# Performance work log

Measured on AMD Instinct MI355X. Metric: run time of the kernel, lower is better.

The kernel has to match this reference:

```python
import jax, jax.numpy as jnp
import numpy as np

NUM_HEADS = 8
NUM_Q = 64
RANK = 64
DIM = 768
LN_EPS = 1e-5


def setup_inputs() -> dict:
    key = jax.random.key(0)
    ks = jax.random.split(key, 8)
    b, n = 4, 1024
    x = jax.random.normal(ks[0], (b, NUM_Q, DIM), dtype=jnp.float32)
    context = jax.random.normal(ks[1], (b, n, DIM), dtype=jnp.float32)
    s = 0.02
    Wq = jax.random.normal(ks[2], (DIM, DIM), dtype=jnp.float32) * s
    Wk = jax.random.normal(ks[3], (DIM, DIM), dtype=jnp.float32) * s
    Wv1 = jax.random.normal(ks[4], (DIM, NUM_Q * RANK), dtype=jnp.float32) * s
    ln_g = jnp.ones((NUM_Q * RANK,), dtype=jnp.float32)
    ln_b = jnp.zeros((NUM_Q * RANK,), dtype=jnp.float32)
    Wc = jax.random.normal(ks[5], (NUM_Q, RANK, DIM), dtype=jnp.float32) * s
    Wout = jax.random.normal(ks[6], (DIM, DIM), dtype=jnp.float32) * s
    return {"x": x, "context": context, "Wq": Wq, "Wk": Wk, "Wv1": Wv1,
            "ln_g": ln_g, "ln_b": ln_b, "Wc": Wc, "Wout": Wout}


def reference(x, context, Wq, Wk, Wv1, ln_g, ln_b, Wc, Wout):
    b, nq, d = x.shape
    n = context.shape[1]
    h, dh = NUM_HEADS, d // NUM_HEADS

    q = x @ Wq                      # [b, nq, d]
    k = context @ Wk                # [b, n, d]

    # q-aware V: Linear -> LayerNorm(all_q_mid) -> grouped 1x1 conv (per-query rank->d)
    h1 = context @ Wv1              # [b, n, NUM_Q*RANK]
    mu = jnp.mean(h1, axis=-1, keepdims=True)
    var = jnp.var(h1, axis=-1, keepdims=True)
    h1 = (h1 - mu) * jax.lax.rsqrt(var + LN_EPS) * ln_g + ln_b
    vmid = h1.reshape(b, n, NUM_Q, RANK)
    v = jnp.einsum('bnqr,qrd->bqnd', vmid, Wc)   # [b, NUM_Q, n, d]
    # split heads: 'b q n (h dh) -> b h q n dh'
    v = v.reshape(b, NUM_Q, n, h, dh).transpose(0, 3, 1, 2, 4)

    qh = q.reshape(b, nq, h, dh).transpose(0, 2, 1, 3)   # [b,h,nq,dh]
    kh = k.reshape(b, n, h, dh).transpose(0, 2, 1, 3)    # [b,h,n,dh]
    scale = dh ** (-0.25)
    sim = jnp.einsum('bhid,bhjd->bhij', qh * scale, kh * scale)
    attn = jax.nn.softmax(sim, axis=-1)                  # [b,h,nq,n]
    out = jnp.einsum('bhij,bhijd->bhid', attn, v)        # per-query V
    out = out.transpose(0, 2, 1, 3).reshape(b, nq, d)
    return out @ Wout
```

## Files before the change

### kernel.cpp

```cpp
#include <hip/hip_runtime.h>
#include <math.h>

typedef unsigned short ushort_t;
typedef __bf16 bf16x8 __attribute__((ext_vector_type(8)));
typedef float f32x4 __attribute__((ext_vector_type(4)));

__device__ __forceinline__ ushort_t f2b_rne(float f) {
    union { float f; unsigned int u; } c;
    c.f = f;
    unsigned int u = c.u;
    u += 0x7FFFu + ((u >> 16) & 1u);
    return (ushort_t)(u >> 16);
}
__device__ __forceinline__ float b2f(ushort_t v) {
    union { unsigned int u; float f; } c;
    c.u = ((unsigned int)v) << 16;
    return c.f;
}

__device__ __forceinline__ void gl_lds16(const ushort_t* g, ushort_t* l) {
    __builtin_amdgcn_global_load_lds(
        (const __attribute__((address_space(1))) void*)g,
        (__attribute__((address_space(3))) void*)l, 16, 0, 0);
}

__global__ __launch_bounds__(256) void prep(
    const float* __restrict__ x, const float* __restrict__ context,
    const float* __restrict__ Wq, const float* __restrict__ Wk,
    const float* __restrict__ Wv1, const float* __restrict__ Wout,
    ushort_t* __restrict__ x_b, ushort_t* __restrict__ ctx_b,
    ushort_t* __restrict__ Wq_t, ushort_t* __restrict__ Wk_t,
    ushort_t* __restrict__ Wv1_t, ushort_t* __restrict__ Wout_b,
    float* __restrict__ colzero,
    int b, int n) {
    const int t = threadIdx.x;
    const int bid = blockIdx.x;
    const int nb_x = (b * 64 * 768 / 4) / 256;
    const int nb_c = (b * n * 768 / 4) / 256;

    if (bid < nb_x + nb_c) {
        const float* in = (bid < nb_x) ? x : context;
        ushort_t* outp = (bid < nb_x) ? x_b : ctx_b;
        const int i = ((bid < nb_x) ? bid : (bid - nb_x)) * 256 + t;
        float4 v = ((const float4*)in)[i];
        ushort_t o[4] = {f2b_rne(v.x), f2b_rne(v.y), f2b_rne(v.z), f2b_rne(v.w)};
        *(uint2*)&outp[(size_t)i * 4] = *(uint2*)o;
        return;
    }

    int u = bid - nb_x - nb_c;
    if (u >= 1632) {
        const int idx = (u - 1632) * 256 + t;
        ((float4*)colzero)[idx] = make_float4(0.f, 0.f, 0.f, 0.f);
        return;
    }
    if (u >= 1056) {
        const int i = (u - 1056) * 256 + t;
        float4 v = ((const float4*)Wout)[i];
        ushort_t o[4] = {f2b_rne(v.x), f2b_rne(v.y), f2b_rne(v.z), f2b_rne(v.w)};
        *(uint2*)&Wout_b[(size_t)i * 4] = *(uint2*)o;
        return;
    }

    const float* in;
    ushort_t* outp;
    int R = 768, C = 768;
    if (u < 144)        { in = Wq;  outp = Wq_t; }
    else if (u < 288)   { u -= 144; in = Wk;  outp = Wk_t; }
    else                { u -= 288; in = Wv1; outp = Wv1_t; C = 4096; }
    const int ct = C / 64;
    const int c0 = (u % ct) * 64, r0 = (u / ct) * 64;

    __shared__ float tt[64][65];
    const int lr = t >> 4;
    const int lc = (t & 15) * 4;
#pragma unroll
    for (int i = 0; i < 4; i++) {
        const float4 v =
            *(const float4*)&in[(size_t)(r0 + lr + 16 * i) * C + c0 + lc];
        tt[lr + 16 * i][lc + 0] = v.x;
        tt[lr + 16 * i][lc + 1] = v.y;
        tt[lr + 16 * i][lc + 2] = v.z;
        tt[lr + 16 * i][lc + 3] = v.w;
    }
    __syncthreads();
    const int rr = (t & 15) * 4;
    const int cc = t >> 4;
#pragma unroll
    for (int i = 0; i < 4; i++) {
        const int col = cc + 16 * i;
        ushort_t o[4] = {f2b_rne(tt[rr + 0][col]), f2b_rne(tt[rr + 1][col]),
                         f2b_rne(tt[rr + 2][col]), f2b_rne(tt[rr + 3][col])};
        *(uint2*)&outp[(size_t)(c0 + col) * R + r0 + rr] = *(uint2*)o;
    }
}

__device__ __forceinline__ void gemm_tile_big(
    const ushort_t* __restrict__ A, const ushort_t* __restrict__ Bt,
    ushort_t* __restrict__ C, int N, int row0, int col0, ushort_t* lds) {
    constexpr int K = 768;
    constexpr int NSTEP = 24;
    constexpr int SLOT = 512 * 32;

    const int t = threadIdx.x;
    const int lane = t & 63, wave = t >> 6;
    const int quad = lane >> 4, l15 = lane & 15;
    const int wm = (wave >> 2) * 128;
    const int wn = (wave & 3) * 64;

    const int srow = lane >> 2;
    const int sslot = (lane & 3) ^ ((lane >> 3) & 3);
    const ushort_t* gA = A + (size_t)(row0 + wave * 32 + srow) * K + sslot * 8;
    const ushort_t* gB = Bt + (size_t)(col0 + wave * 32 + srow) * K + sslot * 8;
    const int ldsA = wave * 1024;
    const int ldsB = 256 * 32 + wave * 1024;

    const int rslot = (quad ^ ((l15 >> 1) & 3)) * 8;
    const int abase = (wm + l15) * 32 + rslot;
    const int bbase = 256 * 32 + (wn + l15) * 32 + rslot;

    f32x4 acc[8][4] = {};
    bf16x8 af[8], bfr[4];

    auto STAGE_A = [&](int s) {
        const int rg = (s & 3) * SLOT;
        const int ko = s * 32;
        gl_lds16(gA + ko, lds + rg + ldsA);
        gl_lds16(gA + 16 * K + ko, lds + rg + ldsA + 512);
    };
    auto STAGE_B = [&](int s) {
        const int rg = (s & 3) * SLOT;
        const int ko = s * 32;
        gl_lds16(gB + ko, lds + rg + ldsB);
        gl_lds16(gB + 16 * K + ko, lds + rg + ldsB + 512);
    };
    auto READ_B = [&](int s) {
        const ushort_t* p = lds + (s & 3) * SLOT + bbase;
#pragma unroll
        for (int j = 0; j < 4; ++j) bfr[j] = *(const bf16x8*)&p[j * 512];
    };
    auto READ_A_LO = [&](int s) {
        const ushort_t* p = lds + (s & 3) * SLOT + abase;
#pragma unroll
        for (int i = 0; i < 4; ++i) af[i] = *(const bf16x8*)&p[i * 512];
    };
    auto READ_A_HI = [&](int s) {
        const ushort_t* p = lds + (s & 3) * SLOT + abase;
#pragma unroll
        for (int i = 4; i < 8; ++i) af[i] = *(const bf16x8*)&p[i * 512];
    };
    auto MFMA_LO = [&]() {
        __builtin_amdgcn_s_setprio(1);
#pragma unroll
        for (int i = 0; i < 4; ++i)
#pragma unroll
            for (int j = 0; j < 4; ++j)
                acc[i][j] = __builtin_amdgcn_mfma_f32_16x16x32_bf16(
                    af[i], bfr[j], acc[i][j], 0, 0, 0);
        __builtin_amdgcn_s_setprio(0);
    };
    auto MFMA_HI = [&]() {
        __builtin_amdgcn_s_setprio(1);
#pragma unroll
        for (int i = 4; i < 8; ++i)
#pragma unroll
            for (int j = 0; j < 4; ++j)
                acc[i][j] = __builtin_amdgcn_mfma_f32_16x16x32_bf16(
                    af[i], bfr[j], acc[i][j], 0, 0, 0);
        __builtin_amdgcn_s_setprio(0);
    };

    STAGE_A(0); STAGE_B(0);
    STAGE_A(1); STAGE_B(1);
    STAGE_A(2); STAGE_B(2);
    asm volatile("s_waitcnt vmcnt(8)" ::: "memory");
    __builtin_amdgcn_s_barrier();

    for (int s = 0; s < NSTEP - 3; ++s) {
        READ_B(s);
        READ_A_LO(s);
        STAGE_A(s + 3);
        __builtin_amdgcn_sched_barrier(0);
        __builtin_amdgcn_s_barrier();
        asm volatile("s_waitcnt lgkmcnt(0)" ::: "memory");
        __builtin_amdgcn_sched_barrier(0);
        MFMA_LO();
        __builtin_amdgcn_sched_barrier(0);
        __builtin_amdgcn_s_barrier();
        READ_A_HI(s);
        STAGE_B(s + 3);
        asm volatile("s_waitcnt vmcnt(8)" ::: "memory");
        __builtin_amdgcn_sched_barrier(0);
        __builtin_amdgcn_s_barrier();
        asm volatile("s_waitcnt lgkmcnt(0)" ::: "memory");
        __builtin_amdgcn_sched_barrier(0);
        MFMA_HI();
        __builtin_amdgcn_sched_barrier(0);
        __builtin_amdgcn_s_barrier();
    }

    asm volatile("s_waitcnt vmcnt(0)" ::: "memory");
    __builtin_amdgcn_s_barrier();
#pragma unroll
    for (int s = NSTEP - 3; s < NSTEP; ++s) {
        READ_B(s);
        READ_A_LO(s);
        READ_A_HI(s);
        asm volatile("s_waitcnt lgkmcnt(0)" ::: "memory");
        __builtin_amdgcn_sched_barrier(0);
        MFMA_LO();
        MFMA_HI();
    }

#pragma unroll
    for (int i = 0; i < 8; ++i)
#pragma unroll
        for (int j = 0; j < 4; ++j)
#pragma unroll
            for (int r = 0; r < 4; ++r) {
                const int row = row0 + wm + i * 16 + quad * 4 + r;
                const int col = col0 + wn + j * 16 + l15;
                C[(size_t)row * N + col] = f2b_rne(acc[i][j][r]);
            }
}

__device__ __forceinline__ void gemm_tile_small(
    const ushort_t* __restrict__ A, const ushort_t* __restrict__ Bt,
    ushort_t* __restrict__ C, int N, int row0, int col0, ushort_t* lds) {
    constexpr int K = 768;
    constexpr int NSTEP = 24;
    constexpr int SLOT = 256 * 32;

    const int t = threadIdx.x;
    const int lane = t & 63, wave = t >> 6;
    const int quad = lane >> 4, l15 = lane & 15;
    const int wm = (wave >> 2) * 64;
    const int wn = (wave & 3) * 32;

    const int srow = lane >> 2;
    const int sslot = (lane & 3) ^ ((lane >> 3) & 3);
    const ushort_t* gA = A + (size_t)(row0 + wave * 16 + srow) * K + sslot * 8;
    const ushort_t* gB = Bt + (size_t)(col0 + wave * 16 + srow) * K + sslot * 8;
    const int ldsA = wave * 512;
    const int ldsB = 128 * 32 + wave * 512;

    const int rslot = (quad ^ ((l15 >> 1) & 3)) * 8;
    const int abase = (wm + l15) * 32 + rslot;
    const int bbase = 128 * 32 + (wn + l15) * 32 + rslot;

    f32x4 acc[4][2] = {};

    auto STAGE = [&](int s) {
        const int rg = (s & 3) * SLOT;
        const int ko = s * 32;
        gl_lds16(gA + ko, lds + rg + ldsA);
        gl_lds16(gB + ko, lds + rg + ldsB);
    };

    auto COMPUTE = [&](int s) {
        const int rg = (s & 3) * SLOT;
        const ushort_t* pA = lds + rg + abase;
        const ushort_t* pB = lds + rg + bbase;
        bf16x8 af[4], bfr[2];
#pragma unroll
        for (int i = 0; i < 4; ++i) af[i] = *(const bf16x8*)&pA[i * 512];
#pragma unroll
        for (int j = 0; j < 2; ++j) bfr[j] = *(const bf16x8*)&pB[j * 512];
        __builtin_amdgcn_s_setprio(1);
#pragma unroll
        for (int i = 0; i < 4; ++i)
#pragma unroll
            for (int j = 0; j < 2; ++j)
                acc[i][j] = __builtin_amdgcn_mfma_f32_16x16x32_bf16(
                    af[i], bfr[j], acc[i][j], 0, 0, 0);
        __builtin_amdgcn_s_setprio(0);
    };

    STAGE(0); STAGE(1); STAGE(2);

    for (int s = 0; s < NSTEP - 3; ++s) {
        __builtin_amdgcn_sched_barrier(0);
        __builtin_amdgcn_s_barrier();
        STAGE(s + 3);
        asm volatile("s_waitcnt vmcnt(6)" ::: "memory");
        __builtin_amdgcn_s_barrier();
        __builtin_amdgcn_sched_barrier(0);
        COMPUTE(s);
    }
    __builtin_amdgcn_sched_barrier(0);
    __builtin_amdgcn_s_barrier();
    asm volatile("s_waitcnt vmcnt(0)" ::: "memory");
    __builtin_amdgcn_s_barrier();
    __builtin_amdgcn_sched_barrier(0);
    COMPUTE(NSTEP - 3);
    COMPUTE(NSTEP - 2);
    COMPUTE(NSTEP - 1);

#pragma unroll
    for (int i = 0; i < 4; ++i)
#pragma unroll
        for (int j = 0; j < 2; ++j)
#pragma unroll
            for (int r = 0; r < 4; ++r) {
                const int row = row0 + wm + i * 16 + quad * 4 + r;
                const int col = col0 + wn + j * 16 + l15;
                C[(size_t)row * N + col] = f2b_rne(acc[i][j][r]);
            }
}

__global__ __launch_bounds__(512, 2) void gemm_ring(
    const ushort_t* __restrict__ x_b, const ushort_t* __restrict__ ctx_b,
    const ushort_t* __restrict__ Wq_t, const ushort_t* __restrict__ Wk_t,
    const ushort_t* __restrict__ Wv1_t,
    ushort_t* __restrict__ qb, ushort_t* __restrict__ kb,
    ushort_t* __restrict__ h1t, int b, int n) {
    extern __shared__ ushort_t lds[];
    const int Mn = b * n;
    const int M = b * 64;
    const int nbig = 16 * (Mn / 256);
    const int nk = (Mn / 128) * 6;
    int u = blockIdx.x;
    if (u < nbig) {
        gemm_tile_big(Wv1_t, ctx_b, h1t, Mn, (u & 15) * 256, (u >> 4) * 256,
                      lds);
    } else if ((u -= nbig) < nk) {
        const int rt = Mn / 128;
        gemm_tile_small(ctx_b, Wk_t, kb, 768, (u % rt) * 128, (u / rt) * 128,
                        lds);
    } else {
        u -= nk;
        const int rt = M / 128;
        gemm_tile_small(x_b, Wq_t, qb, 768, (u % rt) * 128, (u / rt) * 128,
                        lds);
    }
}

__global__ __launch_bounds__(256) void scores_stats(
    const ushort_t* __restrict__ qb, const ushort_t* __restrict__ kb,
    const ushort_t* __restrict__ h1t, float* __restrict__ S,
    float* __restrict__ colsum, float* __restrict__ colsumsq,
    int b, int n, int Mn) {
    __shared__ ushort_t sb[192 * 104];
    const int t = threadIdx.x;
    const int nsc = b * 8 * (n / 128);

    if (blockIdx.x >= nsc) {
        const int u = blockIdx.x - nsc;
        const int rc = u >> 4;
        const int cc = u & 15;
        const int cg = t & 31;
        const int rg = t >> 5;
        const ushort_t* p =
            h1t + (size_t)(rc * 256 + rg * 32) * Mn + cc * 256 + cg * 8;
        float s[8] = {}, s2[8] = {};
#pragma unroll 4
        for (int r = 0; r < 32; r++) {
            const bf16x8 v = *(const bf16x8*)&p[(size_t)r * Mn];
#pragma unroll
            for (int j = 0; j < 8; j++) {
                const float f = (float)v[j];
                s[j] += f;
                s2[j] += f * f;
            }
        }
        float* red = (float*)sb;
#pragma unroll
        for (int j = 0; j < 8; j++) {
            red[rg * 256 + cg * 8 + j] = s[j];
            red[2048 + rg * 256 + cg * 8 + j] = s2[j];
        }
        __syncthreads();
        float ts = 0.f, ts2 = 0.f;
#pragma unroll
        for (int g = 0; g < 8; g++) {
            ts += red[g * 256 + t];
            ts2 += red[2048 + g * 256 + t];
        }
        atomicAdd(&colsum[cc * 256 + t], ts);
        atomicAdd(&colsumsq[cc * 256 + t], ts2);
        return;
    }

    const int nt = n / 128;
    const int n0 = (blockIdx.x % nt) * 128;
    const int bh = blockIdx.x / nt;
    const int bb = bh >> 3, h = bh & 7;
    const int lane = t & 63, wave = t >> 6;
    const int quad = lane >> 4, l15 = lane & 15;
    const int wm = (wave >> 1) * 32;
    const int wn = (wave & 1) * 64;

    ushort_t* Qs = sb;
    ushort_t* Ks = sb + 64 * 104;

    for (int g = t; g < 768; g += 256) {
        const int r = g / 12, s = g - r * 12;
        *(bf16x8*)&Qs[r * 104 + s * 8] =
            *(const bf16x8*)&qb[(size_t)(bb * 64 + r) * 768 + h * 96 + s * 8];
    }
    for (int g = t; g < 1536; g += 256) {
        const int r = g / 12, s = g - r * 12;
        *(bf16x8*)&Ks[r * 104 + s * 8] =
            *(const bf16x8*)&kb[(size_t)(bb * n + n0 + r) * 768 + h * 96 + s * 8];
    }
    __syncthreads();

    f32x4 acc[2][4] = {};
#pragma unroll
    for (int ks = 0; ks < 3; ks++) {
        bf16x8 af[2], bfr[4];
#pragma unroll
        for (int i = 0; i < 2; i++)
            af[i] = *(const bf16x8*)&Qs[(wm + i * 16 + l15) * 104 + ks * 32 + quad * 8];
#pragma unroll
        for (int j = 0; j < 4; j++)
            bfr[j] = *(const bf16x8*)&Ks[(wn + j * 16 + l15) * 104 + ks * 32 + quad * 8];
#pragma unroll
        for (int i = 0; i < 2; i++)
#pragma unroll
            for (int j = 0; j < 4; j++)
                acc[i][j] = __builtin_amdgcn_mfma_f32_16x16x32_bf16(
                    af[i], bfr[j], acc[i][j], 0, 0, 0);
    }

    const float sc = 0.10206207261596575f;
    float* Sp = S + (size_t)bh * 64 * n;
#pragma unroll
    for (int i = 0; i < 2; i++)
#pragma unroll
        for (int j = 0; j < 4; j++)
#pragma unroll
            for (int r = 0; r < 4; r++) {
                const int row = wm + i * 16 + quad * 4 + r;
                const int col = n0 + wn + j * 16 + l15;
                Sp[(size_t)row * n + col] = acc[i][j][r] * sc;
            }
}

__global__ __launch_bounds__(1024) void attn_fused(
    const float* __restrict__ S, const float* __restrict__ colsum,
    const float* __restrict__ colsumsq, const ushort_t* __restrict__ h1t,
    const float* __restrict__ ln_g, const float* __restrict__ ln_b,
    const float* __restrict__ Wc, const ushort_t* __restrict__ Wout_b,
    float* __restrict__ out, int n, int Mn) {
    const int bq = blockIdx.x;
    const int bb = bq >> 6, qi = bq & 63;
    const int tid = threadIdx.x;
    const int lane = tid & 63, wv = tid >> 6;
    const int quad = lane >> 4, l15 = lane & 15;

    __shared__ ushort_t sW[9 * 1032];
    __shared__ ushort_t sH[64 * 264];
    __shared__ float sl[8], swmu[8];
    __shared__ float pm[16], pl[16], pwm[16];
    __shared__ float sA[512];
    __shared__ float sO[768];

    float* sMu = (float*)sH;
    float* sRs = (float*)sH + 1024;

    for (int i = tid; i < n; i += 1024) {
        const float cs = colsum[bb * n + i];
        const float cq = colsumsq[bb * n + i];
        const float m = cs * (1.0f / 4096.0f);
        sMu[i] = m;
        sRs[i] = rsqrtf(cq * (1.0f / 4096.0f) - m * m + 1e-5f);
    }
    for (int i = tid; i < 1032; i += 1024) sW[8 * 1032 + i] = 0;
    __syncthreads();

    const int h = wv >> 1;
    const int half = wv & 1;
    const int nh = n >> 1;
    const int i0 = half * nh;
    const float* Sp = S + ((size_t)(bb * 8 + h) * 64 + qi) * n;
    {
        float m = -1e30f;
        for (int i = i0 + lane; i < i0 + nh; i += 64) m = fmaxf(m, Sp[i]);
#pragma unroll
        for (int off = 32; off > 0; off >>= 1) m = fmaxf(m, __shfl_down(m, off));
        if (lane == 0) pm[wv] = m;
    }
    __syncthreads();
    const float mh = fmaxf(pm[2 * h], pm[2 * h + 1]);
    {
        float l = 0.f, wm = 0.f;
        for (int i = i0 + lane; i < i0 + nh; i += 64) {
            const float e = expf(Sp[i] - mh);
            const float w = e * sRs[i];
            const ushort_t wb = f2b_rne(w);
            sW[h * 1032 + i] = wb;
            l += e;
            wm += b2f(wb) * sMu[i];
        }
#pragma unroll
        for (int off = 32; off > 0; off >>= 1) {
            l += __shfl_down(l, off);
            wm += __shfl_down(wm, off);
        }
        if (lane == 0) { pl[wv] = l; pwm[wv] = wm; }
    }
    __syncthreads();
    if (tid < 8) {
        sl[tid] = pl[2 * tid] + pl[2 * tid + 1];
        swmu[tid] = pwm[2 * tid] + pwm[2 * tid + 1];
    }

    const int mrow = (l15 < 8 ? l15 : 8) * 1032;
    const int jb = wv & 3;
    const int kg = wv >> 2;
    f32x4 acc = {};
    {
        const ushort_t* hp =
            h1t + (size_t)(qi * 64 + jb * 16 + l15) * Mn + bb * n + kg * 256 +
            quad * 8;
        const ushort_t* wp = sW + mrow + kg * 256 + quad * 8;
#pragma unroll
        for (int ks = 0; ks < 8; ks++) {
            const bf16x8 af = *(const bf16x8*)&wp[ks * 32];
            const bf16x8 bf = *(const bf16x8*)&hp[ks * 32];
            acc = __builtin_amdgcn_mfma_f32_16x16x32_bf16(af, bf, acc, 0, 0, 0);
        }
    }
    __syncthreads();
    float* red = (float*)sH;
    *(f32x4*)&red[(size_t)(wv * 64 + lane) * 4] = acc;
    __syncthreads();

    if (wv < 4) {
        f32x4 a = *(const f32x4*)&red[(size_t)(wv * 64 + lane) * 4];
#pragma unroll
        for (int g = 1; g < 4; g++) {
            const f32x4 p = *(const f32x4*)&red[(size_t)((g * 4 + wv) * 64 + lane) * 4];
#pragma unroll
            for (int r = 0; r < 4; r++) a[r] += p[r];
        }
#pragma unroll
        for (int r = 0; r < 4; r++) {
            const int hh = quad * 4 + r;
            if (hh < 8) {
                const int rr = wv * 16 + l15;
                const int c = qi * 64 + rr;
                sA[hh * 64 + rr] =
                    ln_g[c] * ((a[r] - swmu[hh]) / sl[hh]) + ln_b[c];
            }
        }
    }
    __syncthreads();

    for (int d = tid; d < 768; d += 1024) {
        const int hh = d / 96;
        const float* wp = Wc + (size_t)qi * 49152 + d;
        float a = 0.f;
#pragma unroll
        for (int r = 0; r < 64; r++) a += sA[hh * 64 + r] * wp[(size_t)r * 768];
        sO[d] = b2f(f2b_rne(a));
    }
    __syncthreads();

    float* rbuf = (float*)sH;
    if (tid < 768) {
        const int r0 = tid / 96;
        const int c0 = (tid % 96) * 8;
        const ushort_t* wp = Wout_b + (size_t)(r0 * 96) * 768 + c0;
        float acc8[8] = {};
#pragma unroll 4
        for (int s = 0; s < 96; s++) {
            const float sv = sO[r0 * 96 + s];
            const bf16x8 w8 = *(const bf16x8*)&wp[(size_t)s * 768];
#pragma unroll
            for (int j = 0; j < 8; j++) acc8[j] += sv * (float)w8[j];
        }
#pragma unroll
        for (int j = 0; j < 8; j++) rbuf[r0 * 768 + c0 + j] = acc8[j];
    }
    __syncthreads();
    if (tid < 768) {
        float s = 0.f;
#pragma unroll
        for (int g = 0; g < 8; g++) s += rbuf[g * 768 + tid];
        out[(size_t)bq * 768 + tid] = s;
    }
}

extern "C" void kernel_launch(void* const* d_in, const int* in_sizes, int n_in,
                              void* d_out, int out_size, void* d_ws, size_t ws_size,
                              hipStream_t stream) {
    const float* x       = (const float*)d_in[0];
    const float* context = (const float*)d_in[1];
    const float* Wq      = (const float*)d_in[2];
    const float* Wk      = (const float*)d_in[3];
    const float* Wv1     = (const float*)d_in[4];
    const float* ln_g    = (const float*)d_in[5];
    const float* ln_b    = (const float*)d_in[6];
    const float* Wc      = (const float*)d_in[7];
    const float* Wout    = (const float*)d_in[8];
    float* out = (float*)d_out;

    const int b = in_sizes[0] / (64 * 768);
    const int n = in_sizes[1] / (b * 768);
    const int M  = b * 64;
    const int Mn = b * n;

    float* ws = (float*)d_ws;
    size_t off = 0;
    float* S       = ws + off;  off += (size_t)b * 8 * 64 * n;
    float* colsum  = ws + off;  off += (size_t)Mn;
    float* colsumsq= ws + off;  off += (size_t)Mn;

    ushort_t* us = (ushort_t*)(ws + off);
    size_t uo = 0;
    ushort_t* x_b    = us + uo;  uo += (size_t)M * 768;
    ushort_t* ctx_b  = us + uo;  uo += (size_t)Mn * 768;
    ushort_t* qb     = us + uo;  uo += (size_t)M * 768;
    ushort_t* kb     = us + uo;  uo += (size_t)Mn * 768;
    ushort_t* h1t    = us + uo;  uo += (size_t)Mn * 4096;
    ushort_t* Wq_t   = us + uo;  uo += (size_t)768 * 768;
    ushort_t* Wk_t   = us + uo;  uo += (size_t)768 * 768;
    ushort_t* Wv1_t  = us + uo;  uo += (size_t)4096 * 768;
    ushort_t* Wout_b = us + uo;  uo += (size_t)768 * 768;

    const int nb_x = (M * 768 / 4) / 256;
    const int nb_c = (Mn * 768 / 4) / 256;
    prep<<<nb_x + nb_c + 1640, 256, 0, stream>>>(
        x, context, Wq, Wk, Wv1, Wout, x_b, ctx_b, Wq_t, Wk_t, Wv1_t, Wout_b,
        colsum, b, n);

    const int nbig = 16 * (Mn / 256);
    const int nk = (Mn / 128) * 6;
    const int nq = (M / 128) * 6;
    static bool attr_done = false;
    if (!attr_done) {
        (void)hipFuncSetAttribute(reinterpret_cast<const void*>(&gemm_ring),
                                  hipFuncAttributeMaxDynamicSharedMemorySize,
                                  131072);
        attr_done = true;
    }
    gemm_ring<<<nbig + nk + nq, 512, 131072, stream>>>(
        x_b, ctx_b, Wq_t, Wk_t, Wv1_t, qb, kb, h1t, b, n);

    scores_stats<<<b * 8 * (n / 128) + 256, 256, 0, stream>>>(
        qb, kb, h1t, S, colsum, colsumsq, b, n, Mn);

    attn_fused<<<M, 1024, 0, stream>>>(S, colsum, colsumsq, h1t, ln_g, ln_b,
                                       Wc, Wout_b, out, n, Mn);
}
```

Before: 167.5 us.

## Split attn_fused across head halves with atomic output accumulation

```diff
diff --git a/kernel.cpp b/kernel.cpp
--- a/kernel.cpp
+++ b/kernel.cpp
@@ -32,6 +32,7 @@
     ushort_t* __restrict__ Wq_t, ushort_t* __restrict__ Wk_t,
     ushort_t* __restrict__ Wv1_t, ushort_t* __restrict__ Wout_b,
     float* __restrict__ colzero,
+    float* __restrict__ outz,
     int b, int n) {
     const int t = threadIdx.x;
     const int bid = blockIdx.x;
@@ -49,6 +50,11 @@
     }
 
     int u = bid - nb_x - nb_c;
+    if (u >= 1640) {
+        const int idx = (u - 1640) * 256 + t;
+        ((float4*)outz)[idx] = make_float4(0.f, 0.f, 0.f, 0.f);
+        return;
+    }
     if (u >= 1632) {
         const int idx = (u - 1632) * 256 + t;
         ((float4*)colzero)[idx] = make_float4(0.f, 0.f, 0.f, 0.f);
@@ -437,39 +443,42 @@
             }
 }
 
-__global__ __launch_bounds__(1024) void attn_fused(
+__global__ __launch_bounds__(512) void attn_fused(
     const float* __restrict__ S, const float* __restrict__ colsum,
     const float* __restrict__ colsumsq, const ushort_t* __restrict__ h1t,
     const float* __restrict__ ln_g, const float* __restrict__ ln_b,
     const float* __restrict__ Wc, const ushort_t* __restrict__ Wout_b,
     float* __restrict__ out, int n, int Mn) {
     const int bq = blockIdx.x;
-    const int bb = bq >> 6, qi = bq & 63;
+    const int hb = bq & 1;
+    const int bqi = bq >> 1;
+    const int bb = bqi >> 6, qi = bqi & 63;
     const int tid = threadIdx.x;
     const int lane = tid & 63, wv = tid >> 6;
     const int quad = lane >> 4, l15 = lane & 15;
 
-    __shared__ ushort_t sW[9 * 1032];
-    __shared__ ushort_t sH[64 * 264];
-    __shared__ float sl[8], swmu[8];
-    __shared__ float pm[16], pl[16], pwm[16];
-    __shared__ float sA[512];
-    __shared__ float sO[768];
-
-    float* sMu = (float*)sH;
-    float* sRs = (float*)sH + 1024;
-
-    for (int i = tid; i < n; i += 1024) {
+    __shared__ ushort_t sW[5 * 1032];
+    __shared__ float sOv[3072];
+    __shared__ float sl[4], swmu[4];
+    __shared__ float pm[8], pl[8], pwm[8];
+    __shared__ float sA[256];
+    __shared__ float sO[384];
+
+    float* sMu = sOv;
+    float* sRs = sOv + 1024;
+
+    for (int i = tid; i < n; i += 512) {
         const float cs = colsum[bb * n + i];
         const float cq = colsumsq[bb * n + i];
         const float m = cs * (1.0f / 4096.0f);
         sMu[i] = m;
         sRs[i] = rsqrtf(cq * (1.0f / 4096.0f) - m * m + 1e-5f);
     }
-    for (int i = tid; i < 1032; i += 1024) sW[8 * 1032 + i] = 0;
-    __syncthreads();
-
-    const int h = wv >> 1;
+    for (int i = tid; i < 1032; i += 512) sW[4 * 1032 + i] = 0;
+    __syncthreads();
+
+    const int hl = wv >> 1;
+    const int h = hb * 4 + hl;
     const int half = wv & 1;
     const int nh = n >> 1;
     const int i0 = half * nh;
@@ -482,14 +491,14 @@
         if (lane == 0) pm[wv] = m;
     }
     __syncthreads();
-    const float mh = fmaxf(pm[2 * h], pm[2 * h + 1]);
+    const float mh = fmaxf(pm[2 * hl], pm[2 * hl + 1]);
     {
         float l = 0.f, wm = 0.f;
         for (int i = i0 + lane; i < i0 + nh; i += 64) {
             const float e = expf(Sp[i] - mh);
             const float w = e * sRs[i];
             const ushort_t wb = f2b_rne(w);
-            sW[h * 1032 + i] = wb;
+            sW[hl * 1032 + i] = wb;
             l += e;
             wm += b2f(wb) * sMu[i];
         }
@@ -501,68 +510,67 @@
         if (lane == 0) { pl[wv] = l; pwm[wv] = wm; }
     }
     __syncthreads();
-    if (tid < 8) {
+    if (tid < 4) {
         sl[tid] = pl[2 * tid] + pl[2 * tid + 1];
         swmu[tid] = pwm[2 * tid] + pwm[2 * tid + 1];
     }
 
-    const int mrow = (l15 < 8 ? l15 : 8) * 1032;
+    const int mrow = (l15 < 4 ? l15 : 4) * 1032;
     const int jb = wv & 3;
     const int kg = wv >> 2;
     f32x4 acc = {};
     {
         const ushort_t* hp =
-            h1t + (size_t)(qi * 64 + jb * 16 + l15) * Mn + bb * n + kg * 256 +
+            h1t + (size_t)(qi * 64 + jb * 16 + l15) * Mn + bb * n + kg * 512 +
             quad * 8;
-        const ushort_t* wp = sW + mrow + kg * 256 + quad * 8;
-#pragma unroll
-        for (int ks = 0; ks < 8; ks++) {
+        const ushort_t* wp = sW + mrow + kg * 512 + quad * 8;
+#pragma unroll
+        for (int ks = 0; ks < 16; ks++) {
             const bf16x8 af = *(const bf16x8*)&wp[ks * 32];
             const bf16x8 bf = *(const bf16x8*)&hp[ks * 32];
             acc = __builtin_amdgcn_mfma_f32_16x16x32_bf16(af, bf, acc, 0, 0, 0);
         }
     }
     __syncthreads();
-    float* red = (float*)sH;
+    float* red = sOv;
     *(f32x4*)&red[(size_t)(wv * 64 + lane) * 4] = acc;
     __syncthreads();
 
     if (wv < 4) {
         f32x4 a = *(const f32x4*)&red[(size_t)(wv * 64 + lane) * 4];
-#pragma unroll
-        for (int g = 1; g < 4; g++) {
-            const f32x4 p = *(const f32x4*)&red[(size_t)((g * 4 + wv) * 64 + lane) * 4];
-#pragma unroll
-            for (int r = 0; r < 4; r++) a[r] += p[r];
-        }
+        const f32x4 p = *(const f32x4*)&red[(size_t)((wv + 4) * 64 + lane) * 4];
+#pragma unroll
+        for (int r = 0; r < 4; r++) a[r] += p[r];
 #pragma unroll
         for (int r = 0; r < 4; r++) {
-            const int hh = quad * 4 + r;
-            if (hh < 8) {
+            const int hhl = quad * 4 + r;
+            if (hhl < 4) {
                 const int rr = wv * 16 + l15;
                 const int c = qi * 64 + rr;
-                sA[hh * 64 + rr] =
-                    ln_g[c] * ((a[r] - swmu[hh]) / sl[hh]) + ln_b[c];
+                sA[hhl * 64 + rr] =
+                    ln_g[c] * ((a[r] - swmu[hhl]) / sl[hhl]) + ln_b[c];
             }
         }
     }
     __syncthreads();
 
-    for (int d = tid; d < 768; d += 1024) {
-        const int hh = d / 96;
+    if (tid < 384) {
+        const int d = hb * 384 + tid;
+        const int hhl = tid / 96;
         const float* wp = Wc + (size_t)qi * 49152 + d;
         float a = 0.f;
 #pragma unroll
-        for (int r = 0; r < 64; r++) a += sA[hh * 64 + r] * wp[(size_t)r * 768];
-        sO[d] = b2f(f2b_rne(a));
-    }
-    __syncthreads();
-
-    float* rbuf = (float*)sH;
-    if (tid < 768) {
+        for (int r = 0; r < 64; r++) a += sA[hhl * 64 + r] * wp[(size_t)r * 768];
+        sO[tid] = b2f(f2b_rne(a));
+    }
+    __syncthreads();
+
+    float* rbuf = sOv;
+    if (tid < 384) {
         const int r0 = tid / 96;
         const int c0 = (tid % 96) * 8;
-        const ushort_t* wp = Wout_b + (size_t)(r0 * 96) * 768 + c0;
+        const ushort_t* wp =
+            Wout_b + (size_t)(hb * 384 + r0 * 96) * 768 + c0;
         float acc8[8] = {};
 #pragma unroll 4
         for (int s = 0; s < 96; s++) {
@@ -575,11 +583,11 @@
         for (int j = 0; j < 8; j++) rbuf[r0 * 768 + c0 + j] = acc8[j];
     }
     __syncthreads();
-    if (tid < 768) {
+    for (int dout = tid; dout < 768; dout += 512) {
         float s = 0.f;
 #pragma unroll
-        for (int g = 0; g < 8; g++) s += rbuf[g * 768 + tid];
-        out[(size_t)bq * 768 + tid] = s;
+        for (int g = 0; g < 4; g++) s += rbuf[g * 768 + dout];
+        atomicAdd(&out[(size_t)bqi * 768 + dout], s);
     }
 }
 
@@ -622,9 +630,9 @@
 
     const int nb_x = (M * 768 / 4) / 256;
     const int nb_c = (Mn * 768 / 4) / 256;
-    prep<<<nb_x + nb_c + 1640, 256, 0, stream>>>(
+    prep<<<nb_x + nb_c + 1832, 256, 0, stream>>>(
         x, context, Wq, Wk, Wv1, Wout, x_b, ctx_b, Wq_t, Wk_t, Wv1_t, Wout_b,
-        colsum, b, n);
+        colsum, out, b, n);
 
     const int nbig = 16 * (Mn / 256);
     const int nk = (Mn / 128) * 6;
@@ -642,6 +650,6 @@
     scores_stats<<<b * 8 * (n / 128) + 256, 256, 0, stream>>>(
         qb, kb, h1t, S, colsum, colsumsq, b, n, Mn);
 
-    attn_fused<<<M, 1024, 0, stream>>>(S, colsum, colsumsq, h1t, ln_g, ln_b,
-                                       Wc, Wout_b, out, n, Mn);
-}
+    attn_fused<<<M * 2, 512, 0, stream>>>(S, colsum, colsumsq, h1t,
+                                          ln_g, ln_b, Wc, Wout_b, out, n, Mn);
+}
```

Measured after the change: 177.7 us. 1.06x slower.
